# Optimization experiments

Hardware: AMD Instinct MI355X
Metric: run time of the kernel (lower is better)

Reference implementation:

```python
import jax, jax.numpy as jnp
import numpy as np

B, T, C = 4, 2048, 1024
H, G = 16, 4            # n_head, n_groups (GQA)
D = C // H              # head_dim = 64
NEG_INF = -1e30


def setup_inputs() -> dict:
    key = jax.random.key(0)
    k1, k2, k3, k4 = jax.random.split(key, 4)
    x = jax.random.normal(k1, (B, T, C), dtype=jnp.float32)
    Wq = jax.random.normal(k2, (C, C), dtype=jnp.float32) * 0.02
    Wkv = jax.random.normal(k3, (2 * G * D, C), dtype=jnp.float32) * 0.02
    Wproj = jax.random.normal(k4, (C, C), dtype=jnp.float32) * 0.02
    b_proj = jnp.zeros((C,), dtype=jnp.float32)
    return {"x": x, "Wq": Wq, "Wkv": Wkv, "Wproj": Wproj, "b_proj": b_proj}


def reference(x, Wq, Wkv, Wproj, b_proj):
    # q projection: [B,T,C] -> [B,H,T,D]
    q = (x @ Wq.T).reshape(B, T, H, D).transpose(0, 2, 1, 3)
    # fused kv projection -> split into k,v each [B,G,T,D]
    kv = x @ Wkv.T
    k = kv[..., : G * D].reshape(B, T, G, D).transpose(0, 2, 1, 3)
    v = kv[..., G * D :].reshape(B, T, G, D).transpose(0, 2, 1, 3)
    # torch .repeat tiles groups: head h uses kv group h % G
    k = jnp.tile(k, (1, H // G, 1, 1))  # [B,H,T,D]
    v = jnp.tile(v, (1, H // G, 1, 1))
    scale = 1.0 / jnp.sqrt(jnp.asarray(D, dtype=x.dtype))
    scores = jnp.einsum("bhqd,bhkd->bhqk", q, k) * scale  # [B,H,T,T]
    causal = jnp.tril(jnp.ones((T, T), dtype=bool))
    scores = jnp.where(causal, scores, NEG_INF)
    att = jax.nn.softmax(scores, axis=-1)
    y = jnp.einsum("bhqk,bhkd->bhqd", att, v)  # [B,H,T,D]
    y = y.transpose(0, 2, 1, 3).reshape(B, T, C)
    return y @ Wproj.T + b_proj
```

## Files before the change

### kernel.cpp

```cpp
#include <hip/hip_runtime.h>
#include <math.h>
#include <stdint.h>

#define B_ 4
#define T_ 2048
#define C_ 1024
#define H_ 16
#define G_ 4
#define D_ 64
#define KVC_ 512
#define QKV_ 1536
#define KOFF_ 1024
#define VOFF_ 1280

typedef unsigned short u16;
typedef short bf16x8 __attribute__((ext_vector_type(8)));
typedef float f32x4 __attribute__((ext_vector_type(4)));

__device__ __forceinline__ u16 f2bf(float f) {
  uint32_t u = __builtin_bit_cast(uint32_t, f);
  u += 0x7fffu + ((u >> 16) & 1u);
  return (u16)(u >> 16);
}

__device__ __forceinline__ void gload16(const void* g, void* l) {
  __builtin_amdgcn_global_load_lds((const __attribute__((address_space(1))) void*)g,
                                   (__attribute__((address_space(3))) void*)l, 16, 0, 0);
}

__global__ __launch_bounds__(256)
void cvt_bf16(const float* __restrict__ s, u16* __restrict__ d, int n4, float scale) {
  int i = blockIdx.x * 256 + threadIdx.x;
  const int stride = gridDim.x * 256;
  for (; i < n4; i += stride) {
    const float4 v = ((const float4*)s)[i];
    uint2 o;
    o.x = (uint32_t)f2bf(v.x * scale) | ((uint32_t)f2bf(v.y * scale) << 16);
    o.y = (uint32_t)f2bf(v.z * scale) | ((uint32_t)f2bf(v.w * scale) << 16);
    ((uint2*)d)[i] = o;
  }
}

template <int OUTF32>
__global__ __launch_bounds__(256)
void gemm_bf16(const u16* __restrict__ A, const u16* __restrict__ W,
               const float* __restrict__ bias, void* __restrict__ outp,
               int N, int K) {
  __shared__ __align__(16) u16 As[128 * 32];
  __shared__ __align__(16) u16 Ws[128 * 32];
  const int tid = threadIdx.x;
  const int l = tid & 63, w = tid >> 6;
  const int lhi = l >> 4, llo = l & 15;
  const int wr = w >> 1, wc = w & 1;
  const int m0 = blockIdx.x * 128, n0 = blockIdx.y * 128;

  const u16* a_src = A + (size_t)(m0 + 32 * w + (l >> 2)) * K + 8 * (l & 3);
  const u16* w_src = W + (size_t)(n0 + 32 * w + (l >> 2)) * K + 8 * (l & 3);
  u16* asl = As + 1024 * w;
  u16* wsl = Ws + 1024 * w;

  const f32x4 zero4 = {0.f, 0.f, 0.f, 0.f};
  f32x4 acc[4][4];
#pragma unroll
  for (int i = 0; i < 4; ++i)
#pragma unroll
    for (int j = 0; j < 4; ++j) acc[i][j] = zero4;

  for (int k0 = 0; k0 < K; k0 += 32) {
    __syncthreads();
    gload16(a_src + k0, asl);
    gload16(a_src + k0 + 16 * K, asl + 512);
    gload16(w_src + k0, wsl);
    gload16(w_src + k0 + 16 * K, wsl + 512);
    __syncthreads();
    bf16x8 af[4], wf[4];
#pragma unroll
    for (int mt = 0; mt < 4; ++mt)
      af[mt] = *(const bf16x8*)(As + (wr * 64 + mt * 16 + llo) * 32 + lhi * 8);
#pragma unroll
    for (int nt = 0; nt < 4; ++nt)
      wf[nt] = *(const bf16x8*)(Ws + (wc * 64 + nt * 16 + llo) * 32 + lhi * 8);
#pragma unroll
    for (int mt = 0; mt < 4; ++mt)
#pragma unroll
      for (int nt = 0; nt < 4; ++nt)
        acc[mt][nt] = __builtin_amdgcn_mfma_f32_16x16x32_bf16(af[mt], wf[nt], acc[mt][nt], 0, 0, 0);
  }

#pragma unroll
  for (int mt = 0; mt < 4; ++mt)
#pragma unroll
    for (int nt = 0; nt < 4; ++nt)
#pragma unroll
      for (int r = 0; r < 4; ++r) {
        const int row = m0 + wr * 64 + mt * 16 + 4 * lhi + r;
        const int col = n0 + wc * 64 + nt * 16 + llo;
        if (OUTF32)
          ((float*)outp)[(size_t)row * N + col] = acc[mt][nt][r] + bias[col];
        else
          ((u16*)outp)[(size_t)row * N + col] = f2bf(acc[mt][nt][r]);
      }
}

__global__ __launch_bounds__(512)
void attn_kernel(const u16* __restrict__ QKVb, u16* __restrict__ Yb) {
  const int qtb = 15 - blockIdx.x;
  const int bh = blockIdx.y;
  const int b = bh >> 4, h = bh & 15, g = h & (G_ - 1);
  const int tid = threadIdx.x;
  const int l = tid & 63, w = tid >> 6;
  const int lhi = l >> 4, llo = l & 15, l7 = l & 7;

  __shared__ __align__(16) u16 Ks[2][64 * 64];
  __shared__ __align__(16) u16 Vt[2][64 * 64];
  __shared__ __align__(16) u16 Ps[8][16 * 64];

  const int q0 = qtb * 128;
  const int qrow = q0 + 16 * w + llo;
  const u16* qptr = QKVb + (size_t)(b * T_ + qrow) * QKV_ + h * D_ + 8 * lhi;
  const bf16x8 qf0 = *(const bf16x8*)(qptr);
  const bf16x8 qf1 = *(const bf16x8*)(qptr + 32);

  const f32x4 zero4 = {0.f, 0.f, 0.f, 0.f};
  f32x4 o[4];
#pragma unroll
  for (int i = 0; i < 4; ++i) o[i] = zero4;
  float m_s = -__builtin_inff();
  float l_s = 0.f;

  const int skr = tid >> 3;
  const int ksrc_off = 8 * ((tid & 7) ^ (skr & 7));
  const int vkr = 2 * (tid >> 4);
  const int vd4 = 4 * (tid & 15);
  u16* Pw = Ps[w];
  const int rbase = 4 * lhi;
  const int qmax_w = q0 + 16 * w + 15;
  const int ntiles = 2 * qtb + 2;

  {
    const int kv0 = b * T_;
    gload16(QKVb + (size_t)(kv0 + skr) * QKV_ + KOFF_ + g * D_ + ksrc_off,
            Ks[0] + 512 * w);
    const u16* vsrc = QKVb + (size_t)(kv0 + vkr) * QKV_ + VOFF_ + g * D_ + vd4;
    const uint2 a = *(const uint2*)vsrc;
    const uint2 c = *(const uint2*)(vsrc + QKV_);
    const u16* p0 = (const u16*)&a;
    const u16* p1 = (const u16*)&c;
#pragma unroll
    for (int i = 0; i < 4; ++i) {
      const int d = vd4 + i;
      const uint32_t val = (uint32_t)p0[i] | ((uint32_t)p1[i] << 16);
      const int p = (vkr >> 3) ^ (d & 7) ^ ((d >> 3) & 7);
      *(uint32_t*)((char*)Vt[0] + d * 128 + (p << 4) + (vkr & 7) * 2) = val;
    }
  }
  __syncthreads();

  int cur = 0;
  for (int kt = 0; kt < ntiles; ++kt) {
    const bool have_next = (kt + 1) < ntiles;
    uint2 vr0, vr1;
    if (have_next) {
      const int kv0n = b * T_ + (kt + 1) * 64;
      gload16(QKVb + (size_t)(kv0n + skr) * QKV_ + KOFF_ + g * D_ + ksrc_off,
              Ks[cur ^ 1] + 512 * w);
      const u16* vsrc = QKVb + (size_t)(kv0n + vkr) * QKV_ + VOFF_ + g * D_ + vd4;
      vr0 = *(const uint2*)vsrc;
      vr1 = *(const uint2*)(vsrc + QKV_);
    }

    if (kt * 64 <= qmax_w) {
      f32x4 st[4];
#pragma unroll
      for (int mt = 0; mt < 4; ++mt) st[mt] = zero4;
#pragma unroll
      for (int mt = 0; mt < 4; ++mt) {
        const int krow = 16 * mt + llo;
        const u16* kb = Ks[cur] + krow * 64;
        const bf16x8 kf0 = *(const bf16x8*)(kb + ((lhi ^ l7) << 3));
        const bf16x8 kf1 = *(const bf16x8*)(kb + (((lhi + 4) ^ l7) << 3));
        st[mt] = __builtin_amdgcn_mfma_f32_16x16x32_bf16(kf0, qf0, st[mt], 0, 0, 0);
        st[mt] = __builtin_amdgcn_mfma_f32_16x16x32_bf16(kf1, qf1, st[mt], 0, 0, 0);
      }
      if (kt * 64 + 63 > q0 + 16 * w) {
#pragma unroll
        for (int mt = 0; mt < 4; ++mt)
#pragma unroll
          for (int r = 0; r < 4; ++r) {
            const int kr_g = kt * 64 + 16 * mt + rbase + r;
            if (kr_g > qrow) st[mt][r] = -__builtin_inff();
          }
      }
      float mloc = -__builtin_inff();
#pragma unroll
      for (int mt = 0; mt < 4; ++mt)
#pragma unroll
        for (int r = 0; r < 4; ++r) mloc = fmaxf(mloc, st[mt][r]);
      mloc = fmaxf(mloc, __shfl_xor(mloc, 16));
      mloc = fmaxf(mloc, __shfl_xor(mloc, 32));
      const float mnew = fmaxf(m_s, mloc);
      const float corr = __expf(m_s - mnew);
      float ls = 0.f;
#pragma unroll
      for (int mt = 0; mt < 4; ++mt)
#pragma unroll
        for (int r = 0; r < 4; ++r) {
          const float e = __expf(st[mt][r] - mnew);
          st[mt][r] = e;
          ls += e;
        }
      ls += __shfl_xor(ls, 16);
      ls += __shfl_xor(ls, 32);
      l_s = l_s * corr + ls;
      m_s = mnew;
      float c4[4];
#pragma unroll
      for (int r = 0; r < 4; ++r) c4[r] = __shfl(corr, rbase + r);
#pragma unroll
      for (int nt = 0; nt < 4; ++nt)
#pragma unroll
        for (int r = 0; r < 4; ++r) o[nt][r] *= c4[r];

#pragma unroll
      for (int mt = 0; mt < 4; ++mt)
#pragma unroll
        for (int pr = 0; pr < 2; ++pr) {
          const int kr0 = 16 * mt + rbase + 2 * pr;
          const uint32_t val = (uint32_t)f2bf(st[mt][2 * pr]) |
                               ((uint32_t)f2bf(st[mt][2 * pr + 1]) << 16);
          *(uint32_t*)((char*)Pw + llo * 128 + (((kr0 >> 3) ^ l7) << 4) +
                       (kr0 & 7) * 2) = val;
        }
#pragma unroll
      for (int ks = 0; ks < 2; ++ks) {
        const bf16x8 pf = *(const bf16x8*)(Pw + llo * 64 + (((lhi + 4 * ks) ^ l7) << 3));
#pragma unroll
        for (int nt = 0; nt < 4; ++nt) {
          const int d_l = 16 * nt + llo;
          const int fd = l7 ^ ((2 * nt + (llo >> 3)) & 7);
          const bf16x8 vf = *(const bf16x8*)(Vt[cur] + d_l * 64 +
                                             (((lhi + 4 * ks) ^ fd) << 3));
          o[nt] = __builtin_amdgcn_mfma_f32_16x16x32_bf16(pf, vf, o[nt], 0, 0, 0);
        }
      }
    }

    if (have_next) {
      const u16* p0 = (const u16*)&vr0;
      const u16* p1 = (const u16*)&vr1;
#pragma unroll
      for (int i = 0; i < 4; ++i) {
        const int d = vd4 + i;
        const uint32_t val = (uint32_t)p0[i] | ((uint32_t)p1[i] << 16);
        const int p = (vkr >> 3) ^ (d & 7) ^ ((d >> 3) & 7);
        *(uint32_t*)((char*)Vt[cur ^ 1] + d * 128 + (p << 4) + (vkr & 7) * 2) = val;
      }
    }
    __syncthreads();
    cur ^= 1;
  }

  const float invl = 1.f / l_s;
  float i4[4];
#pragma unroll
  for (int r = 0; r < 4; ++r) i4[r] = __shfl(invl, rbase + r);
#pragma unroll
  for (int nt = 0; nt < 4; ++nt)
#pragma unroll
    for (int r = 0; r < 4; ++r) {
      const int qg = q0 + 16 * w + rbase + r;
      const int d = 16 * nt + llo;
      Yb[(size_t)(b * T_ + qg) * C_ + h * D_ + d] = f2bf(o[nt][r] * i4[r]);
    }
}

extern "C" void kernel_launch(void* const* d_in, const int* in_sizes, int n_in,
                              void* d_out, int out_size, void* d_ws, size_t ws_size,
                              hipStream_t stream) {
  (void)in_sizes; (void)n_in; (void)out_size; (void)ws_size;
  const float* x     = (const float*)d_in[0];
  const float* Wq    = (const float*)d_in[1];
  const float* Wkv   = (const float*)d_in[2];
  const float* Wproj = (const float*)d_in[3];
  const float* bproj = (const float*)d_in[4];
  float* out = (float*)d_out;

  const size_t M = (size_t)B_ * T_;
  u16* xb    = (u16*)d_ws;
  u16* QKVb  = xb + M * C_;
  u16* wpb   = QKVb + M * QKV_;
  u16* wqkv  = (u16*)d_out;
  u16* Yb    = xb;

  dim3 blk(256);
  cvt_bf16<<<2048, blk, 0, stream>>>(x, xb, (int)(M * C_ / 4), 1.f);
  cvt_bf16<<<512, blk, 0, stream>>>(Wq, wqkv, C_ * C_ / 4, 0.125f);
  cvt_bf16<<<256, blk, 0, stream>>>(Wkv, wqkv + (size_t)C_ * C_, KVC_ * C_ / 4, 1.f);
  gemm_bf16<0><<<dim3(64, 12), blk, 0, stream>>>(xb, wqkv, nullptr, QKVb, QKV_, C_);
  attn_kernel<<<dim3(16, 64), dim3(512), 0, stream>>>(QKVb, Yb);
  cvt_bf16<<<512, blk, 0, stream>>>(Wproj, wpb, C_ * C_ / 4, 1.f);
  gemm_bf16<1><<<dim3(64, 8), blk, 0, stream>>>(Yb, wpb, bproj, out, C_, C_);
}
```

Before: 307.2 us.

## Use exp2 softmax with lazy rescaling, deferred row sums, and MFMA priority hints

Folds log2(e) into the Q weight scale so softmax uses exp2f instead of __expf. The running max is only updated, and the output rescaled, when some lane's new max exceeds the old one by more than 8, which skips most correction work. Row-sum shuffles move out of the loop into a single reduction at the end. The change also uses the hardware packed bf16 convert instead of manual rounding and raises wave priority around the MFMA sections. Risks are larger exponent ranges (up to 2^8) and slightly different rounding.

```diff
diff --git a/kernel.cpp b/kernel.cpp
--- a/kernel.cpp
+++ b/kernel.cpp
@@ -126,7 +126,7 @@
 #pragma unroll
   for (int i = 0; i < 4; ++i) o[i] = zero4;
   float m_s = -__builtin_inff();
-  float l_s = 0.f;
+  float l_p = 0.f;
 
   const int skr = tid >> 3;
   const int ksrc_off = 8 * ((tid & 7) ^ (skr & 7));
@@ -173,6 +173,7 @@
       f32x4 st[4];
 #pragma unroll
       for (int mt = 0; mt < 4; ++mt) st[mt] = zero4;
+      __builtin_amdgcn_s_setprio(1);
 #pragma unroll
       for (int mt = 0; mt < 4; ++mt) {
         const int krow = 16 * mt + llo;
@@ -182,6 +183,7 @@
         st[mt] = __builtin_amdgcn_mfma_f32_16x16x32_bf16(kf0, qf0, st[mt], 0, 0, 0);
         st[mt] = __builtin_amdgcn_mfma_f32_16x16x32_bf16(kf1, qf1, st[mt], 0, 0, 0);
       }
+      __builtin_amdgcn_s_setprio(0);
       if (kt * 64 + 63 > q0 + 16 * w) {
 #pragma unroll
         for (int mt = 0; mt < 4; ++mt)
@@ -191,46 +193,48 @@
             if (kr_g > qrow) st[mt][r] = -__builtin_inff();
           }
       }
-      float mloc = -__builtin_inff();
+      float mx[4];
 #pragma unroll
       for (int mt = 0; mt < 4; ++mt)
-#pragma unroll
-        for (int r = 0; r < 4; ++r) mloc = fmaxf(mloc, st[mt][r]);
+        mx[mt] = fmaxf(fmaxf(st[mt][0], st[mt][1]), fmaxf(st[mt][2], st[mt][3]));
+      float mloc = fmaxf(fmaxf(mx[0], mx[1]), fmaxf(mx[2], mx[3]));
       mloc = fmaxf(mloc, __shfl_xor(mloc, 16));
       mloc = fmaxf(mloc, __shfl_xor(mloc, 32));
-      const float mnew = fmaxf(m_s, mloc);
-      const float corr = __expf(m_s - mnew);
-      float ls = 0.f;
+      if (!__all(mloc - m_s <= 8.0f)) {
+        const float mnew = fmaxf(m_s, mloc);
+        const float corr = exp2f(m_s - mnew);
+        l_p *= corr;
+        float c4[4];
+#pragma unroll
+        for (int r = 0; r < 4; ++r) c4[r] = __shfl(corr, rbase + r);
+#pragma unroll
+        for (int nt = 0; nt < 4; ++nt)
+#pragma unroll
+          for (int r = 0; r < 4; ++r) o[nt][r] *= c4[r];
+        m_s = mnew;
+      }
 #pragma unroll
       for (int mt = 0; mt < 4; ++mt)
 #pragma unroll
-        for (int r = 0; r < 4; ++r) {
-          const float e = __expf(st[mt][r] - mnew);
-          st[mt][r] = e;
-          ls += e;
-        }
-      ls += __shfl_xor(ls, 16);
-      ls += __shfl_xor(ls, 32);
-      l_s = l_s * corr + ls;
-      m_s = mnew;
-      float c4[4];
-#pragma unroll
-      for (int r = 0; r < 4; ++r) c4[r] = __shfl(corr, rbase + r);
-#pragma unroll
-      for (int nt = 0; nt < 4; ++nt)
-#pragma unroll
-        for (int r = 0; r < 4; ++r) o[nt][r] *= c4[r];
+        for (int r = 0; r < 4; ++r) st[mt][r] = exp2f(st[mt][r] - m_s);
+      float s4[4];
+#pragma unroll
+      for (int mt = 0; mt < 4; ++mt)
+        s4[mt] = (st[mt][0] + st[mt][1]) + (st[mt][2] + st[mt][3]);
+      l_p += (s4[0] + s4[1]) + (s4[2] + s4[3]);
 
 #pragma unroll
       for (int mt = 0; mt < 4; ++mt)
 #pragma unroll
         for (int pr = 0; pr < 2; ++pr) {
           const int kr0 = 16 * mt + rbase + 2 * pr;
-          const uint32_t val = (uint32_t)f2bf(st[mt][2 * pr]) |
-                               ((uint32_t)f2bf(st[mt][2 * pr + 1]) << 16);
+          uint32_t val;
+          asm("v_cvt_pk_bf16_f32 %0, %1, %2"
+              : "=v"(val) : "v"(st[mt][2 * pr]), "v"(st[mt][2 * pr + 1]));
           *(uint32_t*)((char*)Pw + llo * 128 + (((kr0 >> 3) ^ l7) << 4) +
                        (kr0 & 7) * 2) = val;
         }
+      __builtin_amdgcn_s_setprio(1);
 #pragma unroll
       for (int ks = 0; ks < 2; ++ks) {
         const bf16x8 pf = *(const bf16x8*)(Pw + llo * 64 + (((lhi + 4 * ks) ^ l7) << 3));
@@ -243,6 +247,7 @@
           o[nt] = __builtin_amdgcn_mfma_f32_16x16x32_bf16(pf, vf, o[nt], 0, 0, 0);
         }
       }
+      __builtin_amdgcn_s_setprio(0);
     }
 
     if (have_next) {
@@ -260,6 +265,9 @@
     cur ^= 1;
   }
 
+  float l_s = l_p;
+  l_s += __shfl_xor(l_s, 16);
+  l_s += __shfl_xor(l_s, 32);
   const float invl = 1.f / l_s;
   float i4[4];
 #pragma unroll
@@ -294,7 +302,7 @@
 
   dim3 blk(256);
   cvt_bf16<<<2048, blk, 0, stream>>>(x, xb, (int)(M * C_ / 4), 1.f);
-  cvt_bf16<<<512, blk, 0, stream>>>(Wq, wqkv, C_ * C_ / 4, 0.125f);
+  cvt_bf16<<<512, blk, 0, stream>>>(Wq, wqkv, C_ * C_ / 4, 0.125f * 1.44269504f);
   cvt_bf16<<<256, blk, 0, stream>>>(Wkv, wqkv + (size_t)C_ * C_, KVC_ * C_ / 4, 1.f);
   gemm_bf16<0><<<dim3(64, 12), blk, 0, stream>>>(xb, wqkv, nullptr, QKVb, QKV_, C_);
   attn_kernel<<<dim3(16, 64), dim3(512), 0, stream>>>(QKVb, Yb);
```

After: 309.5 us. Within noise of the previous version (+0.8%).
